# Kernel optimization log

Measured on AMD Instinct MI355X. Metric: run time of the kernel, lower is better.

The kernel has to match this reference:

```python
import jax, jax.numpy as jnp
import numpy as np

BS, NC, Nc, D_n = 8, 256, 128, 64
ALPHA, HS, HM = 2, 256, 128
GAMMA_MAX = 0.5
EPS = 1e-6


def setup_inputs() -> dict:
    key = jax.random.key(0)
    ks = jax.random.split(key, 12)
    f = jax.random.normal
    return {
        "x": f(ks[0], (BS, NC, D_n), jnp.float32),
        "h": f(ks[1], (BS, NC, Nc, D_n), jnp.float32) * 0.1,
        "W": f(ks[2], (BS, NC, Nc, Nc), jnp.float32) * (Nc ** -0.5),
        "decay": jax.random.uniform(ks[3], (BS, NC, Nc), jnp.float32),
        "hebbian": f(ks[4], (BS, NC, Nc, Nc), jnp.float32) * 0.01,
        "neuron_id": f(ks[5], (NC, Nc, D_n), jnp.float32) * (D_n ** -0.5),
        "state_w1": f(ks[6], (HS, 2 * D_n), jnp.float32) * ((2 * D_n) ** -0.5),
        "state_b1": jnp.zeros((HS,), jnp.float32),
        "state_w2": f(ks[7], (D_n, HS), jnp.float32) * (HS ** -0.5),
        "state_b2": jnp.zeros((D_n,), jnp.float32),
        "msg_w1": f(ks[8], (HM, D_n), jnp.float32) * (D_n ** -0.5),
        "msg_b1": jnp.zeros((HM,), jnp.float32),
        "msg_w2": f(ks[9], (D_n, HM), jnp.float32) * (HM ** -0.5),
        "msg_b2": jnp.zeros((D_n,), jnp.float32),
        "inject_w": f(ks[10], (NC, ALPHA * D_n, D_n), jnp.float32) * (D_n ** -0.5),
        "inject_b": jnp.zeros((NC, ALPHA * D_n), jnp.float32),
        "W_decay_logit": jnp.full((NC, Nc), -3.0, jnp.float32),
        "decay_gamma_logit": jnp.full((NC, Nc), -3.0, jnp.float32),
        "hebbian_decay_logit": jnp.full((NC, Nc), 2.0, jnp.float32),
    }


def _rms_norm(v):
    # F.rms_norm over the last (Nc) axis, no affine weight
    return v * jax.lax.rsqrt(jnp.mean(v * v, axis=-1, keepdims=True) + EPS)


def reference(x, h, W, decay, hebbian, neuron_id,
              state_w1, state_b1, state_w2, state_b2,
              msg_w1, msg_b1, msg_w2, msg_b2,
              inject_w, inject_b,
              W_decay_logit, decay_gamma_logit, hebbian_decay_logit):
    B = x.shape[0]
    # per-cell injection of external input into the first ALPHA neurons
    inj = jnp.einsum('bcd,cad->bca', x, inject_w) + inject_b   # [B,NC,ALPHA*D_n]
    h = h.at[:, :, :ALPHA, :].add(inj.reshape(B, NC, ALPHA, D_n))
    h_id = h + neuron_id                                       # identity embedding broadcast
    # per-neuron message MLP (tanh hidden)
    m = jnp.tanh(jnp.einsum('bcnd,hd->bcnh', h_id, msg_w1) + msg_b1)
    m = jnp.einsum('bcnh,dh->bcnd', m, msg_w2) + msg_b2        # [B,NC,Nc,D_n]
    # Hebbian-weighted adjacency message passing: small per-cell matmul W @ m
    agg = jnp.einsum('bcij,bcjd->bcid', W, m)
    # state update MLP on concat(state, aggregated message)
    s = jnp.tanh(jnp.einsum('bcnd,hd->bcnh',
                            jnp.concatenate([h_id, agg], axis=-1), state_w1) + state_b1)
    dh = jnp.einsum('bcnh,dh->bcnd', s, state_w2) + state_b2
    # gated decay of per-neuron state
    dg = GAMMA_MAX * jax.nn.sigmoid(decay_gamma_logit)         # [NC,Nc]
    decay_new = (1.0 - dg) * decay + dg * jax.nn.sigmoid(jnp.mean(dh, axis=-1))
    h_new = (1.0 - decay_new[..., None]) * h + decay_new[..., None] * jnp.tanh(dh)
    # Hebbian outer-product plasticity
    hg = GAMMA_MAX * jax.nn.sigmoid(hebbian_decay_logit)
    outer = jnp.einsum('bcid,bcjd->bcij', h_new, m) / D_n
    hebbian_new = (1.0 - hg[..., None]) * hebbian + hg[..., None] * outer
    # decayed adjacency update + rms-norm over the incoming-edge axis
    wg = GAMMA_MAX * jax.nn.sigmoid(W_decay_logit)
    W_new = _rms_norm((1.0 - wg[..., None]) * W + wg[..., None] * hebbian_new)
    return (h_new, m, W_new, decay_new, hebbian_new)
```

## Files before the change

kernel.cpp:

```cpp
#include <hip/hip_runtime.h>
#include <hip/hip_bf16.h>


#define NCELL 256

typedef __attribute__((ext_vector_type(8))) short bf16x8;
typedef __attribute__((ext_vector_type(4))) float f32x4;
typedef __attribute__((ext_vector_type(4))) unsigned short u16x4;

#define MFMA(a, b, c) __builtin_amdgcn_mfma_f32_16x16x32_bf16((a), (b), (c), 0, 0, 0)

__device__ __forceinline__ unsigned short f2bf(float f) {
    return __builtin_bit_cast(unsigned short, __float2bfloat16(f));
}
__device__ __forceinline__ float frcp(float x) { return __builtin_amdgcn_rcpf(x); }
__device__ __forceinline__ float sigm(float v) { return frcp(1.0f + __expf(-v)); }
__device__ __forceinline__ float ftanh(float x) {
    float e = __expf(2.0f * x);
    return 1.0f - 2.0f * frcp(e + 1.0f);
}

__device__ __forceinline__ int swzg(int col, int row) {
    return (((col >> 3) ^ (row & 7)) << 3) | (col & 7);
}
__device__ __forceinline__ int swb(int row, int col) {
    return row * 32 + ((((col >> 3) ^ row) & 3) << 3) + (col & 7);
}

__global__ void cvt_w(const float* __restrict__ a, const float* __restrict__ b,
                      const float* __restrict__ c, const float* __restrict__ d,
                      unsigned short* __restrict__ dst) {
    int i = blockIdx.x * 256 + threadIdx.x;
    if (i < 8192) {
        int row = i >> 6, col = i & 63;
        dst[row * 64 + swzg(col, row)] = f2bf(a[i]);
    } else if (i < 16384) {
        int j = i - 8192;
        int row = j >> 7, col = j & 127;
        dst[8192 + row * 128 + swzg(col, row)] = f2bf(b[j]);
    } else if (i < 49152) {
        dst[i] = f2bf(c[i - 16384]);
    } else {
        int j = i - 49152;
        int row = j >> 8, col = j & 255;
        dst[49152 + row * 256 + swzg(col, row)] = f2bf(d[j]);
    }
}

__global__ __launch_bounds__(512, 4)
void cell_kernel(const float* __restrict__ x, const float* __restrict__ h,
                 const float* __restrict__ W, const float* __restrict__ decay,
                 const float* __restrict__ nid,
                 const float* __restrict__ sb1, const float* __restrict__ sb2,
                 const float* __restrict__ mb1, const float* __restrict__ mb2,
                 const float* __restrict__ injw, const float* __restrict__ injb,
                 const float* __restrict__ dgl,
                 const unsigned short* __restrict__ wbf,
                 float* __restrict__ out) {
    const int c    = blockIdx.x >> 1;
    const int half = blockIdx.x & 1;
    const int tid  = threadIdx.x;
    const int wv   = tid >> 6;
    const int lane = tid & 63;
    const int lr = lane & 15;
    const int lg = lane >> 4;
    const int row0 = wv * 16;

    float* out_h = out;
    float* out_m = out + 16777216;
    float* out_d = out + 67108864;

    __shared__ alignas(16) unsigned short dual_s[8192];
    __shared__ alignas(16) unsigned short w2m_s[8192];
    __shared__ alignas(16) unsigned short w2s_s[16384];
    __shared__ alignas(16) unsigned short hbuf_all[4096];
    __shared__ float inj_s[128];
    unsigned short* hbuf = hbuf_all + wv * 512;

    {
        const uint4* s2m = (const uint4*)(wbf + 8192);
        const uint4* s2s = (const uint4*)(wbf + 49152);
        uint4* d2m = (uint4*)w2m_s;
        uint4* d2s = (uint4*)w2s_s;
        #pragma unroll
        for (int i = 0; i < 2; ++i) d2m[tid + i * 512] = s2m[tid + i * 512];
        #pragma unroll
        for (int i = 0; i < 4; ++i) d2s[tid + i * 512] = s2s[tid + i * 512];
    }

    float nv[2][8];
    {
        const float* nr = nid + (size_t)(c * 128 + row0 + lr) * 64;
        #pragma unroll
        for (int ks = 0; ks < 2; ++ks) {
            float4 n0 = *(const float4*)(nr + ks * 32 + lg * 8);
            float4 n1 = *(const float4*)(nr + ks * 32 + lg * 8 + 4);
            nv[ks][0] = n0.x; nv[ks][1] = n0.y; nv[ks][2] = n0.z; nv[ks][3] = n0.w;
            nv[ks][4] = n1.x; nv[ks][5] = n1.y; nv[ks][6] = n1.z; nv[ks][7] = n1.w;
        }
    }

    const unsigned short* w1s_g = wbf + 16384;

    for (int bb = 0; bb < 4; ++bb) {
        const int b = half * 4 + bb;
        const int cell = b * NCELL + c;

        __syncthreads();

        {
            const uint4* s1m = (const uint4*)wbf;
            uint4* d1 = (uint4*)dual_s;
            #pragma unroll
            for (int i = 0; i < 2; ++i) d1[tid + i * 512] = s1m[tid + i * 512];
        }
        if (wv == 0) {
            const float* xr = x + cell * 64;
            const float* i0 = injw + (c * 128 + lane) * 64;
            const float* i1 = i0 + 64 * 64;
            float acc0 = injb[c * 128 + lane];
            float acc1 = injb[c * 128 + 64 + lane];
            #pragma unroll
            for (int d4 = 0; d4 < 16; ++d4) {
                float4 xv = ((const float4*)xr)[d4];
                float4 aa = ((const float4*)i0)[d4];
                float4 ab = ((const float4*)i1)[d4];
                acc0 += aa.x * xv.x + aa.y * xv.y + aa.z * xv.z + aa.w * xv.w;
                acc1 += ab.x * xv.x + ab.y * xv.y + ab.z * xv.z + ab.w * xv.w;
            }
            inj_s[lane] = acc0;
            inj_s[64 + lane] = acc1;
        }
        __syncthreads();

        bf16x8 aH[2];
        {
            const float* hr = h + (size_t)(cell * 128 + row0 + lr) * 64;
            #pragma unroll
            for (int ks = 0; ks < 2; ++ks) {
                float4 a0 = *(const float4*)(hr + ks * 32 + lg * 8);
                float4 a1 = *(const float4*)(hr + ks * 32 + lg * 8 + 4);
                float v[8] = {a0.x, a0.y, a0.z, a0.w, a1.x, a1.y, a1.z, a1.w};
                unsigned short us[8];
                #pragma unroll
                for (int j = 0; j < 8; ++j) {
                    float hv = v[j] + nv[ks][j];
                    if (row0 + lr < 2) hv += inj_s[(row0 + lr) * 64 + ks * 32 + lg * 8 + j];
                    us[j] = f2bf(hv);
                }
                aH[ks] = *(bf16x8*)us;
            }
        }

        f32x4 accM[4];
        #pragma unroll
        for (int dt = 0; dt < 4; ++dt) accM[dt] = (f32x4){0.f, 0.f, 0.f, 0.f};
        #pragma unroll
        for (int ch = 0; ch < 4; ++ch) {
            f32x4 accH[2];
            accH[0] = (f32x4){0.f, 0.f, 0.f, 0.f};
            accH[1] = (f32x4){0.f, 0.f, 0.f, 0.f};
            #pragma unroll
            for (int ks = 0; ks < 2; ++ks)
                #pragma unroll
                for (int ht = 0; ht < 2; ++ht) {
                    const int wrow = ch * 32 + ht * 16 + lr;
                    bf16x8 bw = *(const bf16x8*)&dual_s[wrow * 64 + swzg(ks * 32 + lg * 8, wrow)];
                    accH[ht] = MFMA(aH[ks], bw, accH[ht]);
                }
            #pragma unroll
            for (int ht = 0; ht < 2; ++ht) {
                float b1v = mb1[ch * 32 + ht * 16 + lr];
                #pragma unroll
                for (int r = 0; r < 4; ++r)
                    hbuf[swb(lg * 4 + r, ht * 16 + lr)] = f2bf(ftanh(accH[ht][r] + b1v));
            }
            bf16x8 aM = *(const bf16x8*)&hbuf[swb(lr, lg * 8)];
            #pragma unroll
            for (int dt = 0; dt < 4; ++dt) {
                const int wrow = dt * 16 + lr;
                bf16x8 bw = *(const bf16x8*)&w2m_s[wrow * 128 + swzg(ch * 32 + lg * 8, wrow)];
                accM[dt] = MFMA(aM, bw, accM[dt]);
            }
        }
        unsigned short us_m[4][4];
        #pragma unroll
        for (int dt = 0; dt < 4; ++dt) {
            float b2v = mb2[dt * 16 + lr];
            #pragma unroll
            for (int r = 0; r < 4; ++r) {
                float mv = accM[dt][r] + b2v;
                out_m[(size_t)(cell * 128 + row0 + lg * 4 + r) * 64 + dt * 16 + lr] = mv;
                us_m[dt][r] = f2bf(mv);
            }
        }
        __syncthreads();

        #pragma unroll
        for (int dt = 0; dt < 4; ++dt)
            #pragma unroll
            for (int r = 0; r < 4; ++r) {
                const int d = dt * 16 + lr;
                dual_s[d * 128 + swzg(row0 + lg * 4 + r, d)] = us_m[dt][r];
            }
        __syncthreads();

        f32x4 accA[4];
        #pragma unroll
        for (int dt = 0; dt < 4; ++dt) accA[dt] = (f32x4){0.f, 0.f, 0.f, 0.f};
        {
            const float* Wr = W + (size_t)cell * 16384 + (row0 + lr) * 128;
            #pragma unroll
            for (int ks = 0; ks < 4; ++ks) {
                float4 wa = *(const float4*)(Wr + ks * 32 + lg * 8);
                float4 wb = *(const float4*)(Wr + ks * 32 + lg * 8 + 4);
                unsigned short uw[8] = {f2bf(wa.x), f2bf(wa.y), f2bf(wa.z), f2bf(wa.w),
                                        f2bf(wb.x), f2bf(wb.y), f2bf(wb.z), f2bf(wb.w)};
                bf16x8 aW = *(bf16x8*)uw;
                #pragma unroll
                for (int dt = 0; dt < 4; ++dt) {
                    const int mrow = dt * 16 + lr;
                    bf16x8 bm = *(const bf16x8*)&dual_s[mrow * 128 + swzg(ks * 32 + lg * 8, mrow)];
                    accA[dt] = MFMA(aW, bm, accA[dt]);
                }
            }
        }
        bf16x8 aG[2];
        #pragma unroll
        for (int p = 0; p < 2; ++p) {
            #pragma unroll
            for (int q = 0; q < 2; ++q)
                #pragma unroll
                for (int r = 0; r < 4; ++r)
                    hbuf[swb(lg * 4 + r, q * 16 + lr)] = f2bf(accA[p * 2 + q][r]);
            aG[p] = *(const bf16x8*)&hbuf[swb(lr, lg * 8)];
        }

        f32x4 accD[4];
        #pragma unroll
        for (int dt = 0; dt < 4; ++dt) accD[dt] = (f32x4){0.f, 0.f, 0.f, 0.f};
        #pragma unroll 2
        for (int ch = 0; ch < 8; ++ch) {
            f32x4 accS[2];
            accS[0] = (f32x4){0.f, 0.f, 0.f, 0.f};
            accS[1] = (f32x4){0.f, 0.f, 0.f, 0.f};
            #pragma unroll
            for (int ks = 0; ks < 4; ++ks) {
                bf16x8 af = (ks < 2) ? aH[ks] : aG[ks - 2];
                #pragma unroll
                for (int ht = 0; ht < 2; ++ht) {
                    bf16x8 bw = *(const bf16x8*)&w1s_g[(ch * 32 + ht * 16 + lr) * 128 + ks * 32 + lg * 8];
                    accS[ht] = MFMA(af, bw, accS[ht]);
                }
            }
            #pragma unroll
            for (int ht = 0; ht < 2; ++ht) {
                float bv = sb1[ch * 32 + ht * 16 + lr];
                #pragma unroll
                for (int r = 0; r < 4; ++r)
                    hbuf[swb(lg * 4 + r, ht * 16 + lr)] = f2bf(ftanh(accS[ht][r] + bv));
            }
            bf16x8 aS = *(const bf16x8*)&hbuf[swb(lr, lg * 8)];
            #pragma unroll
            for (int dt = 0; dt < 4; ++dt) {
                const int wrow = dt * 16 + lr;
                bf16x8 bw = *(const bf16x8*)&w2s_s[wrow * 256 + swzg(ch * 32 + lg * 8, wrow)];
                accD[dt] = MFMA(aS, bw, accD[dt]);
            }
        }

        float dnew[4];
        #pragma unroll
        for (int r = 0; r < 4; ++r) {
            float s = 0.f;
            #pragma unroll
            for (int dt = 0; dt < 4; ++dt) {
                accD[dt][r] += sb2[dt * 16 + lr];
                s += accD[dt][r];
            }
            s += __shfl_xor(s, 1);
            s += __shfl_xor(s, 2);
            s += __shfl_xor(s, 4);
            s += __shfl_xor(s, 8);
            int row = row0 + lg * 4 + r;
            float mean = s * (1.0f / 64.0f);
            float dg = 0.5f * sigm(dgl[c * 128 + row]);
            float dn = (1.0f - dg) * decay[cell * 128 + row] + dg * sigm(mean);
            if (lr == 0) out_d[cell * 128 + row] = dn;
            dnew[r] = dn;
        }
        #pragma unroll
        for (int r = 0; r < 4; ++r) {
            int row = row0 + lg * 4 + r;
            float dn = dnew[r];
            const float* hrr = h + (size_t)(cell * 128 + row) * 64;
            #pragma unroll
            for (int dt = 0; dt < 4; ++dt) {
                int col = dt * 16 + lr;
                float hpost = hrr[col];
                if (row < 2) hpost += inj_s[row * 64 + col];
                float hn = (1.0f - dn) * hpost + dn * ftanh(accD[dt][r]);
                out_h[(size_t)(cell * 128 + row) * 64 + col] = hn;
            }
        }
    }
}

__device__ __forceinline__ int sw64(int row, int col) {
    return row * 64 + ((((col >> 3) ^ row) & 7) << 3) + (col & 7);
}

__global__ __launch_bounds__(256, 4)
void hebb_kernel(const float* __restrict__ W, const float* __restrict__ hebb,
                 const float* __restrict__ wdl, const float* __restrict__ hdl,
                 float* __restrict__ out) {
    const int cell = blockIdx.x;
    const int c = cell & (NCELL - 1);
    const int tid = threadIdx.x;
    const int wv = tid >> 6;
    const int lane = tid & 63;
    const int lr = lane & 15;
    const int lg = lane >> 4;

    const float* hsrc = out + (size_t)cell * 8192;
    const float* msrc = out + 16777216 + (size_t)cell * 8192;
    float* out_W  = out + 33554432;
    float* out_hb = out + 67371008;

    __shared__ alignas(16) unsigned char smem[32768];
    unsigned short* hA = (unsigned short*)smem;
    unsigned short* mB = (unsigned short*)(smem + 16384);

    #pragma unroll
    for (int g = 0; g < 8; ++g) {
        int idx = g * 1024 + tid * 4;
        int row = idx >> 6, col = idx & 63;
        float4 hv = *(const float4*)(hsrc + idx);
        float4 mv = *(const float4*)(msrc + idx);
        u16x4 hu = {f2bf(hv.x), f2bf(hv.y), f2bf(hv.z), f2bf(hv.w)};
        u16x4 mu = {f2bf(mv.x), f2bf(mv.y), f2bf(mv.z), f2bf(mv.w)};
        *(u16x4*)&hA[sw64(row, col)] = hu;
        *(u16x4*)&mB[sw64(row, col)] = mu;
    }
    __syncthreads();

    bf16x8 aO[2][2];
    #pragma unroll
    for (int rt = 0; rt < 2; ++rt)
        #pragma unroll
        for (int ks = 0; ks < 2; ++ks)
            aO[rt][ks] = *(const bf16x8*)&hA[sw64(wv * 32 + rt * 16 + lr, ks * 32 + lg * 8)];

    f32x4 accO[2][8];
    #pragma unroll
    for (int rt = 0; rt < 2; ++rt)
        #pragma unroll
        for (int jt = 0; jt < 8; ++jt)
            accO[rt][jt] = (f32x4){0.f, 0.f, 0.f, 0.f};
    #pragma unroll
    for (int jt = 0; jt < 8; ++jt)
        #pragma unroll
        for (int ks = 0; ks < 2; ++ks) {
            bf16x8 bm = *(const bf16x8*)&mB[sw64(jt * 16 + lr, ks * 32 + lg * 8)];
            #pragma unroll
            for (int rt = 0; rt < 2; ++rt)
                accO[rt][jt] = MFMA(aO[rt][ks], bm, accO[rt][jt]);
        }

    #pragma unroll
    for (int rt = 0; rt < 2; ++rt)
        #pragma unroll
        for (int r = 0; r < 4; ++r) {
            int i = wv * 32 + rt * 16 + lg * 4 + r;
            float hg = 0.5f * sigm(hdl[c * 128 + i]);
            float wg = 0.5f * sigm(wdl[c * 128 + i]);
            const float* hbr = hebb + (size_t)(cell * 128 + i) * 128;
            const float* Wr = W + (size_t)(cell * 128 + i) * 128;
            float* ohb = out_hb + (size_t)(cell * 128 + i) * 128;
            float wpre[8];
            float ss = 0.f;
            #pragma unroll
            for (int jt = 0; jt < 8; ++jt) {
                int j = jt * 16 + lr;
                float o = accO[rt][jt][r] * (1.0f / 64.0f);
                float hbn = (1.0f - hg) * hbr[j] + hg * o;
                ohb[j] = hbn;
                float wp = (1.0f - wg) * Wr[j] + wg * hbn;
                wpre[jt] = wp;
                ss += wp * wp;
            }
            ss += __shfl_xor(ss, 1);
            ss += __shfl_xor(ss, 2);
            ss += __shfl_xor(ss, 4);
            ss += __shfl_xor(ss, 8);
            float scale = rsqrtf(ss * (1.0f / 128.0f) + 1e-6f);
            float* oW = out_W + (size_t)(cell * 128 + i) * 128;
            #pragma unroll
            for (int jt = 0; jt < 8; ++jt)
                oW[jt * 16 + lr] = wpre[jt] * scale;
        }
}

extern "C" void kernel_launch(void* const* d_in, const int* in_sizes, int n_in,
                              void* d_out, int out_size, void* d_ws, size_t ws_size,
                              hipStream_t stream) {
    const float* x    = (const float*)d_in[0];
    const float* h    = (const float*)d_in[1];
    const float* W    = (const float*)d_in[2];
    const float* dec  = (const float*)d_in[3];
    const float* hebb = (const float*)d_in[4];
    const float* nid  = (const float*)d_in[5];
    const float* sw1  = (const float*)d_in[6];
    const float* sb1  = (const float*)d_in[7];
    const float* sw2  = (const float*)d_in[8];
    const float* sb2  = (const float*)d_in[9];
    const float* mw1  = (const float*)d_in[10];
    const float* mb1  = (const float*)d_in[11];
    const float* mw2  = (const float*)d_in[12];
    const float* mb2  = (const float*)d_in[13];
    const float* injw = (const float*)d_in[14];
    const float* injb = (const float*)d_in[15];
    const float* wdl  = (const float*)d_in[16];
    const float* dgl  = (const float*)d_in[17];
    const float* hdl  = (const float*)d_in[18];

    unsigned short* wbf = (unsigned short*)d_ws;

    cvt_w<<<256, 256, 0, stream>>>(mw1, mw2, sw1, sw2, wbf);
    cell_kernel<<<512, 512, 0, stream>>>(x, h, W, dec, nid, sb1, sb2, mb1, mb2,
                                         injw, injb, dgl, wbf, (float*)d_out);
    hebb_kernel<<<2048, 256, 0, stream>>>(W, hebb, wdl, hdl, (float*)d_out);
}
```

Before: 391.3 us.

## Split fused cell kernel into inj, msg, agg and state kernels

The single per-cell kernel becomes separate kernels: an injection GEMV, a message MLP that writes m and a transposed bf16 copy, a W@m aggregation kernel, and a state MLP that reads agg from scratch space in the output buffer. The aim is better parallelism and occupancy, since each stage gets its own grid and the state kernel keeps state_w1 in LDS instead of reading it from global memory. The cost is extra global round-trips for agg, mT and inj, more launches, and reuse of output regions as scratch that the later hebb kernel must overwrite.

Result: slower. 498.4 us (+27.4%).

```diff
diff --git a/kernel.cpp b/kernel.cpp
--- a/kernel.cpp
+++ b/kernel.cpp
@@ -25,6 +25,9 @@
 }
 __device__ __forceinline__ int swb(int row, int col) {
     return row * 32 + ((((col >> 3) ^ row) & 3) << 3) + (col & 7);
+}
+__device__ __forceinline__ int sw64(int row, int col) {
+    return row * 64 + ((((col >> 3) ^ row) & 7) << 3) + (col & 7);
 }
 
 __global__ void cvt_w(const float* __restrict__ a, const float* __restrict__ b,
@@ -39,117 +42,98 @@
         int row = j >> 7, col = j & 127;
         dst[8192 + row * 128 + swzg(col, row)] = f2bf(b[j]);
     } else if (i < 49152) {
-        dst[i] = f2bf(c[i - 16384]);
+        int j = i - 16384;
+        int row = j >> 7, col = j & 127;
+        dst[16384 + row * 128 + swzg(col, row)] = f2bf(c[j]);
     } else {
-        int j = i - 49152;
-        int row = j >> 8, col = j & 255;
-        dst[49152 + row * 256 + swzg(col, row)] = f2bf(d[j]);
-    }
-}
-
-__global__ __launch_bounds__(512, 4)
-void cell_kernel(const float* __restrict__ x, const float* __restrict__ h,
-                 const float* __restrict__ W, const float* __restrict__ decay,
-                 const float* __restrict__ nid,
-                 const float* __restrict__ sb1, const float* __restrict__ sb2,
-                 const float* __restrict__ mb1, const float* __restrict__ mb2,
-                 const float* __restrict__ injw, const float* __restrict__ injb,
-                 const float* __restrict__ dgl,
-                 const unsigned short* __restrict__ wbf,
-                 float* __restrict__ out) {
-    const int c    = blockIdx.x >> 1;
-    const int half = blockIdx.x & 1;
-    const int tid  = threadIdx.x;
-    const int wv   = tid >> 6;
+        dst[i] = f2bf(d[i - 49152]);
+    }
+}
+
+__global__ __launch_bounds__(256, 8)
+void inj_kernel(const float* __restrict__ x, const float* __restrict__ injw,
+                const float* __restrict__ injb, float* __restrict__ inj_ws) {
+    int t = blockIdx.x * 256 + threadIdx.x;
+    int oid = t >> 2;
+    int part = t & 3;
+    int cell = oid >> 7, o = oid & 127, c = cell & (NCELL - 1);
+    const float4* wr = (const float4*)(injw + (c * 128 + o) * 64 + part * 16);
+    const float4* xr = (const float4*)(x + cell * 64 + part * 16);
+    float s = 0.f;
+    #pragma unroll
+    for (int i = 0; i < 4; ++i) {
+        float4 a = wr[i], b = xr[i];
+        s += a.x * b.x + a.y * b.y + a.z * b.z + a.w * b.w;
+    }
+    s += __shfl_xor(s, 1);
+    s += __shfl_xor(s, 2);
+    if (part == 0) inj_ws[oid] = s + injb[c * 128 + o];
+}
+
+__global__ __launch_bounds__(256, 4)
+void msg_kernel(const float* __restrict__ h, const float* __restrict__ nid,
+                const float* __restrict__ mb1, const float* __restrict__ mb2,
+                const unsigned short* __restrict__ wbf,
+                const float* __restrict__ inj_ws,
+                float* __restrict__ out_m, unsigned short* __restrict__ mT_g) {
+    const int tid = threadIdx.x;
+    const int wv = tid >> 6;
     const int lane = tid & 63;
     const int lr = lane & 15;
     const int lg = lane >> 4;
-    const int row0 = wv * 16;
-
-    float* out_h = out;
-    float* out_m = out + 16777216;
-    float* out_d = out + 67108864;
-
-    __shared__ alignas(16) unsigned short dual_s[8192];
+
+    __shared__ alignas(16) unsigned short w1m_s[8192];
     __shared__ alignas(16) unsigned short w2m_s[8192];
-    __shared__ alignas(16) unsigned short w2s_s[16384];
-    __shared__ alignas(16) unsigned short hbuf_all[4096];
-    __shared__ float inj_s[128];
+    __shared__ alignas(16) unsigned short hbuf_all[2048];
     unsigned short* hbuf = hbuf_all + wv * 512;
 
     {
-        const uint4* s2m = (const uint4*)(wbf + 8192);
-        const uint4* s2s = (const uint4*)(wbf + 49152);
-        uint4* d2m = (uint4*)w2m_s;
-        uint4* d2s = (uint4*)w2s_s;
-        #pragma unroll
-        for (int i = 0; i < 2; ++i) d2m[tid + i * 512] = s2m[tid + i * 512];
-        #pragma unroll
-        for (int i = 0; i < 4; ++i) d2s[tid + i * 512] = s2s[tid + i * 512];
-    }
-
-    float nv[2][8];
-    {
-        const float* nr = nid + (size_t)(c * 128 + row0 + lr) * 64;
+        const uint4* s1 = (const uint4*)wbf;
+        const uint4* s2 = (const uint4*)(wbf + 8192);
+        uint4* d1 = (uint4*)w1m_s;
+        uint4* d2 = (uint4*)w2m_s;
+        #pragma unroll
+        for (int i = 0; i < 4; ++i) { d1[tid + i * 256] = s1[tid + i * 256]; }
+        #pragma unroll
+        for (int i = 0; i < 4; ++i) { d2[tid + i * 256] = s2[tid + i * 256]; }
+    }
+    __syncthreads();
+
+    float mb1v[8], mb2v[4];
+    #pragma unroll
+    for (int ch = 0; ch < 4; ++ch)
+        #pragma unroll
+        for (int ht = 0; ht < 2; ++ht)
+            mb1v[ch * 2 + ht] = mb1[ch * 32 + ht * 16 + lr];
+    #pragma unroll
+    for (int dt = 0; dt < 4; ++dt) mb2v[dt] = mb2[dt * 16 + lr];
+
+    const int g0 = blockIdx.x * 16 + wv * 4;
+    for (int g = g0; g < g0 + 4; ++g) {
+        const int row0 = g * 16;
+        const int cell = row0 >> 7;
+        const int arow = row0 + lr;
+        const int nro = arow & 127;
+
+        bf16x8 aH[2];
         #pragma unroll
         for (int ks = 0; ks < 2; ++ks) {
-            float4 n0 = *(const float4*)(nr + ks * 32 + lg * 8);
-            float4 n1 = *(const float4*)(nr + ks * 32 + lg * 8 + 4);
-            nv[ks][0] = n0.x; nv[ks][1] = n0.y; nv[ks][2] = n0.z; nv[ks][3] = n0.w;
-            nv[ks][4] = n1.x; nv[ks][5] = n1.y; nv[ks][6] = n1.z; nv[ks][7] = n1.w;
-        }
-    }
-
-    const unsigned short* w1s_g = wbf + 16384;
-
-    for (int bb = 0; bb < 4; ++bb) {
-        const int b = half * 4 + bb;
-        const int cell = b * NCELL + c;
-
-        __syncthreads();
-
-        {
-            const uint4* s1m = (const uint4*)wbf;
-            uint4* d1 = (uint4*)dual_s;
-            #pragma unroll
-            for (int i = 0; i < 2; ++i) d1[tid + i * 512] = s1m[tid + i * 512];
-        }
-        if (wv == 0) {
-            const float* xr = x + cell * 64;
-            const float* i0 = injw + (c * 128 + lane) * 64;
-            const float* i1 = i0 + 64 * 64;
-            float acc0 = injb[c * 128 + lane];
-            float acc1 = injb[c * 128 + 64 + lane];
-            #pragma unroll
-            for (int d4 = 0; d4 < 16; ++d4) {
-                float4 xv = ((const float4*)xr)[d4];
-                float4 aa = ((const float4*)i0)[d4];
-                float4 ab = ((const float4*)i1)[d4];
-                acc0 += aa.x * xv.x + aa.y * xv.y + aa.z * xv.z + aa.w * xv.w;
-                acc1 += ab.x * xv.x + ab.y * xv.y + ab.z * xv.z + ab.w * xv.w;
-            }
-            inj_s[lane] = acc0;
-            inj_s[64 + lane] = acc1;
-        }
-        __syncthreads();
-
-        bf16x8 aH[2];
-        {
-            const float* hr = h + (size_t)(cell * 128 + row0 + lr) * 64;
-            #pragma unroll
-            for (int ks = 0; ks < 2; ++ks) {
-                float4 a0 = *(const float4*)(hr + ks * 32 + lg * 8);
-                float4 a1 = *(const float4*)(hr + ks * 32 + lg * 8 + 4);
-                float v[8] = {a0.x, a0.y, a0.z, a0.w, a1.x, a1.y, a1.z, a1.w};
-                unsigned short us[8];
-                #pragma unroll
-                for (int j = 0; j < 8; ++j) {
-                    float hv = v[j] + nv[ks][j];
-                    if (row0 + lr < 2) hv += inj_s[(row0 + lr) * 64 + ks * 32 + lg * 8 + j];
-                    us[j] = f2bf(hv);
-                }
-                aH[ks] = *(bf16x8*)us;
-            }
+            const float* hr = h + (size_t)arow * 64 + ks * 32 + lg * 8;
+            const float* nr = nid + (size_t)(arow & 32767) * 64 + ks * 32 + lg * 8;
+            float4 a0 = *(const float4*)hr;
+            float4 a1 = *(const float4*)(hr + 4);
+            float4 n0 = *(const float4*)nr;
+            float4 n1 = *(const float4*)(nr + 4);
+            float v[8] = {a0.x, a0.y, a0.z, a0.w, a1.x, a1.y, a1.z, a1.w};
+            float nn[8] = {n0.x, n0.y, n0.z, n0.w, n1.x, n1.y, n1.z, n1.w};
+            unsigned short us[8];
+            #pragma unroll
+            for (int j = 0; j < 8; ++j) {
+                float hv = v[j] + nn[j];
+                if (nro < 2) hv += inj_ws[cell * 128 + nro * 64 + ks * 32 + lg * 8 + j];
+                us[j] = f2bf(hv);
+            }
+            aH[ks] = *(bf16x8*)us;
         }
 
         f32x4 accM[4];
@@ -165,16 +149,15 @@
                 #pragma unroll
                 for (int ht = 0; ht < 2; ++ht) {
                     const int wrow = ch * 32 + ht * 16 + lr;
-                    bf16x8 bw = *(const bf16x8*)&dual_s[wrow * 64 + swzg(ks * 32 + lg * 8, wrow)];
+                    bf16x8 bw = *(const bf16x8*)&w1m_s[wrow * 64 + swzg(ks * 32 + lg * 8, wrow)];
                     accH[ht] = MFMA(aH[ks], bw, accH[ht]);
                 }
             #pragma unroll
-            for (int ht = 0; ht < 2; ++ht) {
-                float b1v = mb1[ch * 32 + ht * 16 + lr];
+            for (int ht = 0; ht < 2; ++ht)
                 #pragma unroll
                 for (int r = 0; r < 4; ++r)
-                    hbuf[swb(lg * 4 + r, ht * 16 + lr)] = f2bf(ftanh(accH[ht][r] + b1v));
-            }
+                    hbuf[swb(lg * 4 + r, ht * 16 + lr)] =
+                        f2bf(ftanh(accH[ht][r] + mb1v[ch * 2 + ht]));
             bf16x8 aM = *(const bf16x8*)&hbuf[swb(lr, lg * 8)];
             #pragma unroll
             for (int dt = 0; dt < 4; ++dt) {
@@ -183,63 +166,148 @@
                 accM[dt] = MFMA(aM, bw, accM[dt]);
             }
         }
-        unsigned short us_m[4][4];
+
+        const int nrow0 = (row0 & 127) + lg * 4;
         #pragma unroll
         for (int dt = 0; dt < 4; ++dt) {
-            float b2v = mb2[dt * 16 + lr];
+            unsigned short um[4];
             #pragma unroll
             for (int r = 0; r < 4; ++r) {
-                float mv = accM[dt][r] + b2v;
-                out_m[(size_t)(cell * 128 + row0 + lg * 4 + r) * 64 + dt * 16 + lr] = mv;
-                us_m[dt][r] = f2bf(mv);
-            }
-        }
-        __syncthreads();
-
+                float mv = accM[dt][r] + mb2v[dt];
+                out_m[(size_t)(row0 + lg * 4 + r) * 64 + dt * 16 + lr] = mv;
+                um[r] = f2bf(mv);
+            }
+            *(u16x4*)&mT_g[(size_t)cell * 8192 + (dt * 16 + lr) * 128 + nrow0] =
+                *(u16x4*)um;
+        }
+    }
+}
+
+__global__ __launch_bounds__(256, 6)
+void agg_kernel(const float* __restrict__ W, const unsigned short* __restrict__ mT_g,
+                float* __restrict__ agg_ws) {
+    const int cell = blockIdx.x;
+    const int tid = threadIdx.x;
+    const int wv = tid >> 6;
+    const int lane = tid & 63;
+    const int lr = lane & 15;
+    const int lg = lane >> 4;
+
+    const unsigned short* mTc = mT_g + (size_t)cell * 8192;
+    const float* Wbase = W + (size_t)cell * 16384;
+
+    f32x4 accA[2][4];
+    #pragma unroll
+    for (int rt = 0; rt < 2; ++rt)
         #pragma unroll
         for (int dt = 0; dt < 4; ++dt)
-            #pragma unroll
-            for (int r = 0; r < 4; ++r) {
-                const int d = dt * 16 + lr;
-                dual_s[d * 128 + swzg(row0 + lg * 4 + r, d)] = us_m[dt][r];
-            }
-        __syncthreads();
-
-        f32x4 accA[4];
-        #pragma unroll
-        for (int dt = 0; dt < 4; ++dt) accA[dt] = (f32x4){0.f, 0.f, 0.f, 0.f};
-        {
-            const float* Wr = W + (size_t)cell * 16384 + (row0 + lr) * 128;
-            #pragma unroll
-            for (int ks = 0; ks < 4; ++ks) {
-                float4 wa = *(const float4*)(Wr + ks * 32 + lg * 8);
-                float4 wb = *(const float4*)(Wr + ks * 32 + lg * 8 + 4);
-                unsigned short uw[8] = {f2bf(wa.x), f2bf(wa.y), f2bf(wa.z), f2bf(wa.w),
-                                        f2bf(wb.x), f2bf(wb.y), f2bf(wb.z), f2bf(wb.w)};
-                bf16x8 aW = *(bf16x8*)uw;
-                #pragma unroll
-                for (int dt = 0; dt < 4; ++dt) {
-                    const int mrow = dt * 16 + lr;
-                    bf16x8 bm = *(const bf16x8*)&dual_s[mrow * 128 + swzg(ks * 32 + lg * 8, mrow)];
-                    accA[dt] = MFMA(aW, bm, accA[dt]);
-                }
-            }
-        }
-        bf16x8 aG[2];
-        #pragma unroll
-        for (int p = 0; p < 2; ++p) {
-            #pragma unroll
-            for (int q = 0; q < 2; ++q)
-                #pragma unroll
-                for (int r = 0; r < 4; ++r)
-                    hbuf[swb(lg * 4 + r, q * 16 + lr)] = f2bf(accA[p * 2 + q][r]);
-            aG[p] = *(const bf16x8*)&hbuf[swb(lr, lg * 8)];
+            accA[rt][dt] = (f32x4){0.f, 0.f, 0.f, 0.f};
+
+    #pragma unroll
+    for (int ks = 0; ks < 4; ++ks) {
+        bf16x8 bmv[4];
+        #pragma unroll
+        for (int dt = 0; dt < 4; ++dt)
+            bmv[dt] = *(const bf16x8*)&mTc[(dt * 16 + lr) * 128 + ks * 32 + lg * 8];
+        #pragma unroll
+        for (int rt = 0; rt < 2; ++rt) {
+            const float* wr = Wbase + (wv * 32 + rt * 16 + lr) * 128 + ks * 32 + lg * 8;
+            float4 wa = *(const float4*)wr;
+            float4 wb = *(const float4*)(wr + 4);
+            unsigned short uw[8] = {f2bf(wa.x), f2bf(wa.y), f2bf(wa.z), f2bf(wa.w),
+                                    f2bf(wb.x), f2bf(wb.y), f2bf(wb.z), f2bf(wb.w)};
+            bf16x8 aW = *(bf16x8*)uw;
+            #pragma unroll
+            for (int dt = 0; dt < 4; ++dt)
+                accA[rt][dt] = MFMA(aW, bmv[dt], accA[rt][dt]);
+        }
+    }
+    float* adst = agg_ws + (size_t)cell * 8192;
+    #pragma unroll
+    for (int rt = 0; rt < 2; ++rt)
+        #pragma unroll
+        for (int dt = 0; dt < 4; ++dt)
+            #pragma unroll
+            for (int r = 0; r < 4; ++r)
+                adst[(wv * 32 + rt * 16 + lg * 4 + r) * 64 + dt * 16 + lr] = accA[rt][dt][r];
+}
+
+__global__ __launch_bounds__(512, 4)
+void state_kernel(const float* __restrict__ h, const float* __restrict__ nid,
+                  const float* __restrict__ decay,
+                  const float* __restrict__ sb1, const float* __restrict__ sb2,
+                  const float* __restrict__ dgl,
+                  const unsigned short* __restrict__ wbf,
+                  const float* __restrict__ inj_ws, const float* __restrict__ agg_ws,
+                  float* __restrict__ out_h, float* __restrict__ out_d) {
+    const int tid = threadIdx.x;
+    const int wv = tid >> 6;
+    const int lane = tid & 63;
+    const int lr = lane & 15;
+    const int lg = lane >> 4;
+
+    __shared__ alignas(16) unsigned short w1s_s[32768];
+    __shared__ alignas(16) unsigned short hbuf_all[4096];
+    unsigned short* hbuf = hbuf_all + wv * 512;
+
+    {
+        const uint4* s1 = (const uint4*)(wbf + 16384);
+        uint4* d1 = (uint4*)w1s_s;
+        #pragma unroll
+        for (int i = 0; i < 8; ++i) d1[tid + i * 512] = s1[tid + i * 512];
+    }
+    __syncthreads();
+
+    const unsigned short* w2s_g = wbf + 49152;
+
+    float sb1v[16], sb2v[4];
+    #pragma unroll
+    for (int ch = 0; ch < 8; ++ch)
+        #pragma unroll
+        for (int ht = 0; ht < 2; ++ht)
+            sb1v[ch * 2 + ht] = sb1[ch * 32 + ht * 16 + lr];
+    #pragma unroll
+    for (int dt = 0; dt < 4; ++dt) sb2v[dt] = sb2[dt * 16 + lr];
+
+    const int g0 = blockIdx.x * 16 + wv * 2;
+    for (int g = g0; g < g0 + 2; ++g) {
+        const int row0 = g * 16;
+        const int cell = row0 >> 7;
+        const int c = cell & (NCELL - 1);
+        const int arow = row0 + lr;
+        const int nro = arow & 127;
+
+        bf16x8 aH[2], aG[2];
+        #pragma unroll
+        for (int ks = 0; ks < 2; ++ks) {
+            const float* hr = h + (size_t)arow * 64 + ks * 32 + lg * 8;
+            const float* nr = nid + (size_t)(arow & 32767) * 64 + ks * 32 + lg * 8;
+            const float* ar = agg_ws + (size_t)arow * 64 + ks * 32 + lg * 8;
+            float4 a0 = *(const float4*)hr;
+            float4 a1 = *(const float4*)(hr + 4);
+            float4 n0 = *(const float4*)nr;
+            float4 n1 = *(const float4*)(nr + 4);
+            float4 g0v = *(const float4*)ar;
+            float4 g1v = *(const float4*)(ar + 4);
+            float v[8] = {a0.x, a0.y, a0.z, a0.w, a1.x, a1.y, a1.z, a1.w};
+            float nn[8] = {n0.x, n0.y, n0.z, n0.w, n1.x, n1.y, n1.z, n1.w};
+            float gg[8] = {g0v.x, g0v.y, g0v.z, g0v.w, g1v.x, g1v.y, g1v.z, g1v.w};
+            unsigned short uh[8], ug[8];
+            #pragma unroll
+            for (int j = 0; j < 8; ++j) {
+                float hv = v[j] + nn[j];
+                if (nro < 2) hv += inj_ws[cell * 128 + nro * 64 + ks * 32 + lg * 8 + j];
+                uh[j] = f2bf(hv);
+                ug[j] = f2bf(gg[j]);
+            }
+            aH[ks] = *(bf16x8*)uh;
+            aG[ks] = *(bf16x8*)ug;
         }
 
         f32x4 accD[4];
         #pragma unroll
         for (int dt = 0; dt < 4; ++dt) accD[dt] = (f32x4){0.f, 0.f, 0.f, 0.f};
-        #pragma unroll 2
+        #pragma unroll
         for (int ch = 0; ch < 8; ++ch) {
             f32x4 accS[2];
             accS[0] = (f32x4){0.f, 0.f, 0.f, 0.f};
@@ -249,65 +317,54 @@
                 bf16x8 af = (ks < 2) ? aH[ks] : aG[ks - 2];
                 #pragma unroll
                 for (int ht = 0; ht < 2; ++ht) {
-                    bf16x8 bw = *(const bf16x8*)&w1s_g[(ch * 32 + ht * 16 + lr) * 128 + ks * 32 + lg * 8];
+                    const int wrow = ch * 32 + ht * 16 + lr;
+                    bf16x8 bw = *(const bf16x8*)&w1s_s[wrow * 128 + swzg(ks * 32 + lg * 8, wrow)];
                     accS[ht] = MFMA(af, bw, accS[ht]);
                 }
             }
             #pragma unroll
-            for (int ht = 0; ht < 2; ++ht) {
-                float bv = sb1[ch * 32 + ht * 16 + lr];
+            for (int ht = 0; ht < 2; ++ht)
                 #pragma unroll
                 for (int r = 0; r < 4; ++r)
-                    hbuf[swb(lg * 4 + r, ht * 16 + lr)] = f2bf(ftanh(accS[ht][r] + bv));
-            }
+                    hbuf[swb(lg * 4 + r, ht * 16 + lr)] =
+                        f2bf(ftanh(accS[ht][r] + sb1v[ch * 2 + ht]));
             bf16x8 aS = *(const bf16x8*)&hbuf[swb(lr, lg * 8)];
             #pragma unroll
             for (int dt = 0; dt < 4; ++dt) {
-                const int wrow = dt * 16 + lr;
-                bf16x8 bw = *(const bf16x8*)&w2s_s[wrow * 256 + swzg(ch * 32 + lg * 8, wrow)];
+                bf16x8 bw = *(const bf16x8*)&w2s_g[(dt * 16 + lr) * 256 + ch * 32 + lg * 8];
                 accD[dt] = MFMA(aS, bw, accD[dt]);
             }
         }
 
-        float dnew[4];
         #pragma unroll
         for (int r = 0; r < 4; ++r) {
             float s = 0.f;
             #pragma unroll
             for (int dt = 0; dt < 4; ++dt) {
-                accD[dt][r] += sb2[dt * 16 + lr];
+                accD[dt][r] += sb2v[dt];
                 s += accD[dt][r];
             }
             s += __shfl_xor(s, 1);
             s += __shfl_xor(s, 2);
             s += __shfl_xor(s, 4);
             s += __shfl_xor(s, 8);
-            int row = row0 + lg * 4 + r;
+            const int row2 = row0 + lg * 4 + r;
+            const int nro2 = row2 & 127;
             float mean = s * (1.0f / 64.0f);
-            float dg = 0.5f * sigm(dgl[c * 128 + row]);
-            float dn = (1.0f - dg) * decay[cell * 128 + row] + dg * sigm(mean);
-            if (lr == 0) out_d[cell * 128 + row] = dn;
-            dnew[r] = dn;
-        }
-        #pragma unroll
-        for (int r = 0; r < 4; ++r) {
-            int row = row0 + lg * 4 + r;
-            float dn = dnew[r];
-            const float* hrr = h + (size_t)(cell * 128 + row) * 64;
+            float dg = 0.5f * sigm(dgl[c * 128 + nro2]);
+            float dn = (1.0f - dg) * decay[row2] + dg * sigm(mean);
+            if (lr == 0) out_d[row2] = dn;
+            const float* hrr = h + (size_t)row2 * 64;
             #pragma unroll
             for (int dt = 0; dt < 4; ++dt) {
                 int col = dt * 16 + lr;
                 float hpost = hrr[col];
-                if (row < 2) hpost += inj_s[row * 64 + col];
+                if (nro2 < 2) hpost += inj_ws[cell * 128 + nro2 * 64 + col];
                 float hn = (1.0f - dn) * hpost + dn * ftanh(accD[dt][r]);
-                out_h[(size_t)(cell * 128 + row) * 64 + col] = hn;
-            }
-        }
-    }
-}
-
-__device__ __forceinline__ int sw64(int row, int col) {
-    return row * 64 + ((((col >> 3) ^ row) & 7) << 3) + (col & 7);
+                out_h[(size_t)row2 * 64 + col] = hn;
+            }
+        }
+    }
 }
 
 __global__ __launch_bounds__(256, 4)
@@ -424,10 +481,20 @@
     const float* dgl  = (const float*)d_in[17];
     const float* hdl  = (const float*)d_in[18];
 
+    float* out = (float*)d_out;
     unsigned short* wbf = (unsigned short*)d_ws;
+    float* out_m  = out + 16777216;
+    float* agg_ws = out + 33554432;
+    float* out_h  = out;
+    float* out_d  = out + 67108864;
+    float* inj_ws = out + 67371008;
+    unsigned short* mT_g = (unsigned short*)(out + 67371008 + 262144);
 
     cvt_w<<<256, 256, 0, stream>>>(mw1, mw2, sw1, sw2, wbf);
-    cell_kernel<<<512, 512, 0, stream>>>(x, h, W, dec, nid, sb1, sb2, mb1, mb2,
-                                         injw, injb, dgl, wbf, (float*)d_out);
-    hebb_kernel<<<2048, 256, 0, stream>>>(W, hebb, wdl, hdl, (float*)d_out);
-}
+    inj_kernel<<<4096, 256, 0, stream>>>(x, injw, injb, inj_ws);
+    msg_kernel<<<1024, 256, 0, stream>>>(h, nid, mb1, mb2, wbf, inj_ws, out_m, mT_g);
+    agg_kernel<<<2048, 256, 0, stream>>>(W, mT_g, agg_ws);
+    state_kernel<<<1024, 512, 0, stream>>>(h, nid, dec, sb1, sb2, dgl, wbf,
+                                           inj_ws, agg_ws, out_h, out_d);
+    hebb_kernel<<<2048, 256, 0, stream>>>(W, hebb, wdl, hdl, out);
+}
```

## Assign one cell per wave and move injection to a separate kernel

Applied to the files above, without the earlier changes.

Restructures the cell kernel so each wavefront processes a whole cell independently, looping over 8 row tiles, which removes the block-wide __syncthreads between phases. MLP weights are now read straight from global/L2 in bf16 instead of being staged in LDS, and the per-cell input injection is computed by a new standalone kernel into a scratch area of the output buffer. The intent is to cut synchronisation and LDS staging overhead. In exchange, h/neuron_id are reloaded twice, every weight read goes through the cache hierarchy, and the scratch region (the hebbian output area) is overwritten later by the hebbian kernel, which relies on launch ordering.

After: 460.2 us. 17.6% more time.

```diff
diff --git a/kernel.cpp b/kernel.cpp
--- a/kernel.cpp
+++ b/kernel.cpp
@@ -20,142 +20,108 @@
     return 1.0f - 2.0f * frcp(e + 1.0f);
 }
 
-__device__ __forceinline__ int swzg(int col, int row) {
-    return (((col >> 3) ^ (row & 7)) << 3) | (col & 7);
-}
 __device__ __forceinline__ int swb(int row, int col) {
     return row * 32 + ((((col >> 3) ^ row) & 3) << 3) + (col & 7);
+}
+__device__ __forceinline__ int swm(int d, int col) {
+    return d * 128 + ((((col >> 3) ^ (d & 7)) & 15) << 3) + (col & 7);
+}
+__device__ __forceinline__ int sw64(int row, int col) {
+    return row * 64 + ((((col >> 3) ^ row) & 7) << 3) + (col & 7);
 }
 
 __global__ void cvt_w(const float* __restrict__ a, const float* __restrict__ b,
                       const float* __restrict__ c, const float* __restrict__ d,
                       unsigned short* __restrict__ dst) {
     int i = blockIdx.x * 256 + threadIdx.x;
-    if (i < 8192) {
-        int row = i >> 6, col = i & 63;
-        dst[row * 64 + swzg(col, row)] = f2bf(a[i]);
-    } else if (i < 16384) {
-        int j = i - 8192;
-        int row = j >> 7, col = j & 127;
-        dst[8192 + row * 128 + swzg(col, row)] = f2bf(b[j]);
-    } else if (i < 49152) {
-        dst[i] = f2bf(c[i - 16384]);
-    } else {
-        int j = i - 49152;
-        int row = j >> 8, col = j & 255;
-        dst[49152 + row * 256 + swzg(col, row)] = f2bf(d[j]);
+    float v;
+    if (i < 8192) v = a[i];
+    else if (i < 16384) v = b[i - 8192];
+    else if (i < 49152) v = c[i - 16384];
+    else v = d[i - 49152];
+    dst[i] = f2bf(v);
+}
+
+__global__ __launch_bounds__(256, 8)
+void inj_kernel(const float* __restrict__ x, const float* __restrict__ injw,
+                const float* __restrict__ injb, float* __restrict__ inj_ws) {
+    int t = blockIdx.x * 256 + threadIdx.x;
+    int oid = t >> 2;
+    int part = t & 3;
+    int cell = oid >> 7, o = oid & 127, c = cell & (NCELL - 1);
+    const float4* wr = (const float4*)(injw + (c * 128 + o) * 64 + part * 16);
+    const float4* xr = (const float4*)(x + cell * 64 + part * 16);
+    float s = 0.f;
+    #pragma unroll
+    for (int i = 0; i < 4; ++i) {
+        float4 a = wr[i], b = xr[i];
+        s += a.x * b.x + a.y * b.y + a.z * b.z + a.w * b.w;
     }
-}
-
-__global__ __launch_bounds__(512, 4)
-void cell_kernel(const float* __restrict__ x, const float* __restrict__ h,
-                 const float* __restrict__ W, const float* __restrict__ decay,
-                 const float* __restrict__ nid,
-                 const float* __restrict__ sb1, const float* __restrict__ sb2,
-                 const float* __restrict__ mb1, const float* __restrict__ mb2,
-                 const float* __restrict__ injw, const float* __restrict__ injb,
-                 const float* __restrict__ dgl,
-                 const unsigned short* __restrict__ wbf,
-                 float* __restrict__ out) {
-    const int c    = blockIdx.x >> 1;
-    const int half = blockIdx.x & 1;
-    const int tid  = threadIdx.x;
-    const int wv   = tid >> 6;
+    s += __shfl_xor(s, 1);
+    s += __shfl_xor(s, 2);
+    if (part == 0) inj_ws[oid] = s + injb[c * 128 + o];
+}
+
+__global__ __launch_bounds__(256, 2)
+void cell_wave_kernel(const float* __restrict__ h, const float* __restrict__ W,
+                      const float* __restrict__ decay, const float* __restrict__ nid,
+                      const float* __restrict__ sb1, const float* __restrict__ sb2,
+                      const float* __restrict__ mb1, const float* __restrict__ mb2,
+                      const float* __restrict__ dgl,
+                      const unsigned short* __restrict__ wbf,
+                      const float* __restrict__ inj_ws,
+                      float* __restrict__ out_h, float* __restrict__ out_m,
+                      float* __restrict__ out_d) {
+    const int tid = threadIdx.x;
+    const int wv = tid >> 6;
     const int lane = tid & 63;
     const int lr = lane & 15;
     const int lg = lane >> 4;
-    const int row0 = wv * 16;
-
-    float* out_h = out;
-    float* out_m = out + 16777216;
-    float* out_d = out + 67108864;
-
-    __shared__ alignas(16) unsigned short dual_s[8192];
-    __shared__ alignas(16) unsigned short w2m_s[8192];
-    __shared__ alignas(16) unsigned short w2s_s[16384];
-    __shared__ alignas(16) unsigned short hbuf_all[4096];
-    __shared__ float inj_s[128];
-    unsigned short* hbuf = hbuf_all + wv * 512;
-
-    {
-        const uint4* s2m = (const uint4*)(wbf + 8192);
-        const uint4* s2s = (const uint4*)(wbf + 49152);
-        uint4* d2m = (uint4*)w2m_s;
-        uint4* d2s = (uint4*)w2s_s;
-        #pragma unroll
-        for (int i = 0; i < 2; ++i) d2m[tid + i * 512] = s2m[tid + i * 512];
-        #pragma unroll
-        for (int i = 0; i < 4; ++i) d2s[tid + i * 512] = s2s[tid + i * 512];
-    }
-
-    float nv[2][8];
-    {
-        const float* nr = nid + (size_t)(c * 128 + row0 + lr) * 64;
+    const int cell = blockIdx.x * 4 + wv;
+    const int c = cell & (NCELL - 1);
+
+    const unsigned short* w1m = wbf;
+    const unsigned short* w2m = wbf + 8192;
+    const unsigned short* w1s = wbf + 16384;
+    const unsigned short* w2s = wbf + 49152;
+
+    __shared__ alignas(16) unsigned short mT_all[4][8192];
+    __shared__ alignas(16) unsigned short hbuf_all[4][512];
+    unsigned short* mT = mT_all[wv];
+    unsigned short* hbuf = hbuf_all[wv];
+
+    const float* hc = h + (size_t)cell * 8192;
+    const float* nc = nid + (size_t)c * 8192;
+    const float* injc = inj_ws + (size_t)cell * 128;
+
+    #pragma unroll 1
+    for (int rt = 0; rt < 8; ++rt) {
+        const int row = rt * 16 + lr;
+        bf16x8 aH[2];
         #pragma unroll
         for (int ks = 0; ks < 2; ++ks) {
-            float4 n0 = *(const float4*)(nr + ks * 32 + lg * 8);
-            float4 n1 = *(const float4*)(nr + ks * 32 + lg * 8 + 4);
-            nv[ks][0] = n0.x; nv[ks][1] = n0.y; nv[ks][2] = n0.z; nv[ks][3] = n0.w;
-            nv[ks][4] = n1.x; nv[ks][5] = n1.y; nv[ks][6] = n1.z; nv[ks][7] = n1.w;
-        }
-    }
-
-    const unsigned short* w1s_g = wbf + 16384;
-
-    for (int bb = 0; bb < 4; ++bb) {
-        const int b = half * 4 + bb;
-        const int cell = b * NCELL + c;
-
-        __syncthreads();
-
-        {
-            const uint4* s1m = (const uint4*)wbf;
-            uint4* d1 = (uint4*)dual_s;
-            #pragma unroll
-            for (int i = 0; i < 2; ++i) d1[tid + i * 512] = s1m[tid + i * 512];
-        }
-        if (wv == 0) {
-            const float* xr = x + cell * 64;
-            const float* i0 = injw + (c * 128 + lane) * 64;
-            const float* i1 = i0 + 64 * 64;
-            float acc0 = injb[c * 128 + lane];
-            float acc1 = injb[c * 128 + 64 + lane];
-            #pragma unroll
-            for (int d4 = 0; d4 < 16; ++d4) {
-                float4 xv = ((const float4*)xr)[d4];
-                float4 aa = ((const float4*)i0)[d4];
-                float4 ab = ((const float4*)i1)[d4];
-                acc0 += aa.x * xv.x + aa.y * xv.y + aa.z * xv.z + aa.w * xv.w;
-                acc1 += ab.x * xv.x + ab.y * xv.y + ab.z * xv.z + ab.w * xv.w;
-            }
-            inj_s[lane] = acc0;
-            inj_s[64 + lane] = acc1;
-        }
-        __syncthreads();
-
-        bf16x8 aH[2];
-        {
-            const float* hr = h + (size_t)(cell * 128 + row0 + lr) * 64;
-            #pragma unroll
-            for (int ks = 0; ks < 2; ++ks) {
-                float4 a0 = *(const float4*)(hr + ks * 32 + lg * 8);
-                float4 a1 = *(const float4*)(hr + ks * 32 + lg * 8 + 4);
-                float v[8] = {a0.x, a0.y, a0.z, a0.w, a1.x, a1.y, a1.z, a1.w};
-                unsigned short us[8];
-                #pragma unroll
-                for (int j = 0; j < 8; ++j) {
-                    float hv = v[j] + nv[ks][j];
-                    if (row0 + lr < 2) hv += inj_s[(row0 + lr) * 64 + ks * 32 + lg * 8 + j];
-                    us[j] = f2bf(hv);
-                }
-                aH[ks] = *(bf16x8*)us;
-            }
+            const int col = ks * 32 + lg * 8;
+            float4 a0 = *(const float4*)(hc + row * 64 + col);
+            float4 a1 = *(const float4*)(hc + row * 64 + col + 4);
+            float4 n0 = *(const float4*)(nc + row * 64 + col);
+            float4 n1 = *(const float4*)(nc + row * 64 + col + 4);
+            float v[8] = {a0.x, a0.y, a0.z, a0.w, a1.x, a1.y, a1.z, a1.w};
+            float nn[8] = {n0.x, n0.y, n0.z, n0.w, n1.x, n1.y, n1.z, n1.w};
+            unsigned short us[8];
+            #pragma unroll
+            for (int j = 0; j < 8; ++j) {
+                float hv = v[j] + nn[j];
+                if (row < 2) hv += injc[row * 64 + col + j];
+                us[j] = f2bf(hv);
+            }
+            aH[ks] = *(bf16x8*)us;
         }
 
         f32x4 accM[4];
         #pragma unroll
         for (int dt = 0; dt < 4; ++dt) accM[dt] = (f32x4){0.f, 0.f, 0.f, 0.f};
-        #pragma unroll
+
+        #pragma unroll 1
         for (int ch = 0; ch < 4; ++ch) {
             f32x4 accH[2];
             accH[0] = (f32x4){0.f, 0.f, 0.f, 0.f};
@@ -164,8 +130,7 @@
             for (int ks = 0; ks < 2; ++ks)
                 #pragma unroll
                 for (int ht = 0; ht < 2; ++ht) {
-                    const int wrow = ch * 32 + ht * 16 + lr;
-                    bf16x8 bw = *(const bf16x8*)&dual_s[wrow * 64 + swzg(ks * 32 + lg * 8, wrow)];
+                    bf16x8 bw = *(const bf16x8*)&w1m[(ch * 32 + ht * 16 + lr) * 64 + ks * 32 + lg * 8];
                     accH[ht] = MFMA(aH[ks], bw, accH[ht]);
                 }
             #pragma unroll
@@ -178,51 +143,45 @@
             bf16x8 aM = *(const bf16x8*)&hbuf[swb(lr, lg * 8)];
             #pragma unroll
             for (int dt = 0; dt < 4; ++dt) {
-                const int wrow = dt * 16 + lr;
-                bf16x8 bw = *(const bf16x8*)&w2m_s[wrow * 128 + swzg(ch * 32 + lg * 8, wrow)];
+                bf16x8 bw = *(const bf16x8*)&w2m[(dt * 16 + lr) * 128 + ch * 32 + lg * 8];
                 accM[dt] = MFMA(aM, bw, accM[dt]);
             }
         }
-        unsigned short us_m[4][4];
+
+        const int n0c = rt * 16 + lg * 4;
         #pragma unroll
         for (int dt = 0; dt < 4; ++dt) {
             float b2v = mb2[dt * 16 + lr];
+            unsigned short um[4];
             #pragma unroll
             for (int r = 0; r < 4; ++r) {
                 float mv = accM[dt][r] + b2v;
-                out_m[(size_t)(cell * 128 + row0 + lg * 4 + r) * 64 + dt * 16 + lr] = mv;
-                us_m[dt][r] = f2bf(mv);
-            }
-        }
-        __syncthreads();
-
-        #pragma unroll
-        for (int dt = 0; dt < 4; ++dt)
-            #pragma unroll
-            for (int r = 0; r < 4; ++r) {
-                const int d = dt * 16 + lr;
-                dual_s[d * 128 + swzg(row0 + lg * 4 + r, d)] = us_m[dt][r];
-            }
-        __syncthreads();
+                out_m[(size_t)cell * 8192 + (n0c + r) * 64 + dt * 16 + lr] = mv;
+                um[r] = f2bf(mv);
+            }
+            *(u16x4*)&mT[swm(dt * 16 + lr, n0c)] = *(u16x4*)um;
+        }
+    }
+
+    #pragma unroll 1
+    for (int rt = 0; rt < 8; ++rt) {
+        const int row = rt * 16 + lr;
 
         f32x4 accA[4];
         #pragma unroll
         for (int dt = 0; dt < 4; ++dt) accA[dt] = (f32x4){0.f, 0.f, 0.f, 0.f};
-        {
-            const float* Wr = W + (size_t)cell * 16384 + (row0 + lr) * 128;
-            #pragma unroll
-            for (int ks = 0; ks < 4; ++ks) {
-                float4 wa = *(const float4*)(Wr + ks * 32 + lg * 8);
-                float4 wb = *(const float4*)(Wr + ks * 32 + lg * 8 + 4);
-                unsigned short uw[8] = {f2bf(wa.x), f2bf(wa.y), f2bf(wa.z), f2bf(wa.w),
-                                        f2bf(wb.x), f2bf(wb.y), f2bf(wb.z), f2bf(wb.w)};
-                bf16x8 aW = *(bf16x8*)uw;
-                #pragma unroll
-                for (int dt = 0; dt < 4; ++dt) {
-                    const int mrow = dt * 16 + lr;
-                    bf16x8 bm = *(const bf16x8*)&dual_s[mrow * 128 + swzg(ks * 32 + lg * 8, mrow)];
-                    accA[dt] = MFMA(aW, bm, accA[dt]);
-                }
+        #pragma unroll
+        for (int ks = 0; ks < 4; ++ks) {
+            const float* wr = W + (size_t)cell * 16384 + row * 128 + ks * 32 + lg * 8;
+            float4 wa = *(const float4*)wr;
+            float4 wb = *(const float4*)(wr + 4);
+            unsigned short uw[8] = {f2bf(wa.x), f2bf(wa.y), f2bf(wa.z), f2bf(wa.w),
+                                    f2bf(wb.x), f2bf(wb.y), f2bf(wb.z), f2bf(wb.w)};
+            bf16x8 aW = *(bf16x8*)uw;
+            #pragma unroll
+            for (int dt = 0; dt < 4; ++dt) {
+                bf16x8 bm = *(const bf16x8*)&mT[swm(dt * 16 + lr, ks * 32 + lg * 8)];
+                accA[dt] = MFMA(aW, bm, accA[dt]);
             }
         }
         bf16x8 aG[2];
@@ -236,10 +195,30 @@
             aG[p] = *(const bf16x8*)&hbuf[swb(lr, lg * 8)];
         }
 
+        bf16x8 aH[2];
+        #pragma unroll
+        for (int ks = 0; ks < 2; ++ks) {
+            const int col = ks * 32 + lg * 8;
+            float4 a0 = *(const float4*)(hc + row * 64 + col);
+            float4 a1 = *(const float4*)(hc + row * 64 + col + 4);
+            float4 n0 = *(const float4*)(nc + row * 64 + col);
+            float4 n1 = *(const float4*)(nc + row * 64 + col + 4);
+            float v[8] = {a0.x, a0.y, a0.z, a0.w, a1.x, a1.y, a1.z, a1.w};
+            float nn[8] = {n0.x, n0.y, n0.z, n0.w, n1.x, n1.y, n1.z, n1.w};
+            unsigned short us[8];
+            #pragma unroll
+            for (int j = 0; j < 8; ++j) {
+                float hv = v[j] + nn[j];
+                if (row < 2) hv += injc[row * 64 + col + j];
+                us[j] = f2bf(hv);
+            }
+            aH[ks] = *(bf16x8*)us;
+        }
+
         f32x4 accD[4];
         #pragma unroll
         for (int dt = 0; dt < 4; ++dt) accD[dt] = (f32x4){0.f, 0.f, 0.f, 0.f};
-        #pragma unroll 2
+        #pragma unroll 1
         for (int ch = 0; ch < 8; ++ch) {
             f32x4 accS[2];
             accS[0] = (f32x4){0.f, 0.f, 0.f, 0.f};
@@ -249,7 +228,7 @@
                 bf16x8 af = (ks < 2) ? aH[ks] : aG[ks - 2];
                 #pragma unroll
                 for (int ht = 0; ht < 2; ++ht) {
-                    bf16x8 bw = *(const bf16x8*)&w1s_g[(ch * 32 + ht * 16 + lr) * 128 + ks * 32 + lg * 8];
+                    bf16x8 bw = *(const bf16x8*)&w1s[(ch * 32 + ht * 16 + lr) * 128 + ks * 32 + lg * 8];
                     accS[ht] = MFMA(af, bw, accS[ht]);
                 }
             }
@@ -263,13 +242,11 @@
             bf16x8 aS = *(const bf16x8*)&hbuf[swb(lr, lg * 8)];
             #pragma unroll
             for (int dt = 0; dt < 4; ++dt) {
-                const int wrow = dt * 16 + lr;
-                bf16x8 bw = *(const bf16x8*)&w2s_s[wrow * 256 + swzg(ch * 32 + lg * 8, wrow)];
+                bf16x8 bw = *(const bf16x8*)&w2s[(dt * 16 + lr) * 256 + ch * 32 + lg * 8];
                 accD[dt] = MFMA(aS, bw, accD[dt]);
             }
         }
 
-        float dnew[4];
         #pragma unroll
         for (int r = 0; r < 4; ++r) {
             float s = 0.f;
@@ -282,32 +259,21 @@
             s += __shfl_xor(s, 2);
             s += __shfl_xor(s, 4);
             s += __shfl_xor(s, 8);
-            int row = row0 + lg * 4 + r;
+            const int row2 = rt * 16 + lg * 4 + r;
             float mean = s * (1.0f / 64.0f);
-            float dg = 0.5f * sigm(dgl[c * 128 + row]);
-            float dn = (1.0f - dg) * decay[cell * 128 + row] + dg * sigm(mean);
-            if (lr == 0) out_d[cell * 128 + row] = dn;
-            dnew[r] = dn;
-        }
-        #pragma unroll
-        for (int r = 0; r < 4; ++r) {
-            int row = row0 + lg * 4 + r;
-            float dn = dnew[r];
-            const float* hrr = h + (size_t)(cell * 128 + row) * 64;
+            float dg = 0.5f * sigm(dgl[c * 128 + row2]);
+            float dn = (1.0f - dg) * decay[(size_t)cell * 128 + row2] + dg * sigm(mean);
+            if (lr == 0) out_d[(size_t)cell * 128 + row2] = dn;
             #pragma unroll
             for (int dt = 0; dt < 4; ++dt) {
                 int col = dt * 16 + lr;
-                float hpost = hrr[col];
-                if (row < 2) hpost += inj_s[row * 64 + col];
+                float hpost = hc[row2 * 64 + col];
+                if (row2 < 2) hpost += injc[row2 * 64 + col];
                 float hn = (1.0f - dn) * hpost + dn * ftanh(accD[dt][r]);
-                out_h[(size_t)(cell * 128 + row) * 64 + col] = hn;
+                out_h[(size_t)cell * 8192 + row2 * 64 + col] = hn;
             }
         }
     }
-}
-
-__device__ __forceinline__ int sw64(int row, int col) {
-    return row * 64 + ((((col >> 3) ^ row) & 7) << 3) + (col & 7);
 }
 
 __global__ __launch_bounds__(256, 4)
@@ -424,10 +390,16 @@
     const float* dgl  = (const float*)d_in[17];
     const float* hdl  = (const float*)d_in[18];
 
+    float* out = (float*)d_out;
     unsigned short* wbf = (unsigned short*)d_ws;
+    float* out_h  = out;
+    float* out_m  = out + 16777216;
+    float* out_d  = out + 67108864;
+    float* inj_ws = out + 67371008;
 
     cvt_w<<<256, 256, 0, stream>>>(mw1, mw2, sw1, sw2, wbf);
-    cell_kernel<<<512, 512, 0, stream>>>(x, h, W, dec, nid, sb1, sb2, mb1, mb2,
-                                         injw, injb, dgl, wbf, (float*)d_out);
-    hebb_kernel<<<2048, 256, 0, stream>>>(W, hebb, wdl, hdl, (float*)d_out);
-}
+    inj_kernel<<<4096, 256, 0, stream>>>(x, injw, injb, inj_ws);
+    cell_wave_kernel<<<512, 256, 0, stream>>>(h, W, dec, nid, sb1, sb2, mb1, mb2,
+                                              dgl, wbf, inj_ws, out_h, out_m, out_d);
+    hebb_kernel<<<2048, 256, 0, stream>>>(W, hebb, wdl, hdl, out);
+}
```
